# Performance work log

Hardware: AMD Instinct MI355X
Metric: run time of the kernel (lower is better)

The kernel has to match this reference:

```python
import jax, jax.numpy as jnp
import numpy as np

N = 8192
FEAT = 128
HID = 128
EMB = 128
NHEADS = 2
RO_HID = 256
G_EMB = 128
ALPHA = 0.2          # LeakyReLU negative slope
NEG_INF = -9e15      # matches -9000000000000000.0 in the torch source


def _xavier(k, shape, gain=1.0):
    fan_in, fan_out = shape[-2], shape[-1]
    s = gain * np.sqrt(2.0 / (fan_in + fan_out))
    return jax.random.normal(k, shape, jnp.float32) * jnp.float32(s)


def setup_inputs() -> dict:
    key = jax.random.key(0)
    ks = jax.random.split(key, 10)
    adj = jax.random.randint(ks[0], (N, N), 0, 2, jnp.int32)          # dense 0/1 adjacency
    x = jax.random.normal(ks[1], (N, FEAT), jnp.float32)
    W_heads = _xavier(ks[2], (NHEADS, FEAT, HID), gain=1.414)
    a_heads = _xavier(ks[3], (NHEADS, 2 * HID, 1), gain=1.414)
    W_out = _xavier(ks[4], (NHEADS * HID, EMB), gain=1.414)
    a_out = _xavier(ks[5], (2 * EMB, 1), gain=1.414)
    ge_w1 = _xavier(ks[6], (FEAT + EMB, RO_HID))
    ge_b1 = jnp.zeros((RO_HID,), jnp.float32)
    ge_w2 = _xavier(ks[7], (RO_HID, G_EMB))
    ge_b2 = jnp.zeros((G_EMB,), jnp.float32)
    return dict(adj=adj, feature_matrix=x, W_heads=W_heads, a_heads=a_heads,
                W_out=W_out, a_out=a_out, ge_w1=ge_w1, ge_b1=ge_b1,
                ge_w2=ge_w2, ge_b2=ge_b2, supply=0)


def _gat_layer(x, mask, W, a, concat):
    # Faithful to GraphAttentionLayer: e_ij = leakyrelu([Wh_i || Wh_j] @ a).
    # The concat-then-matmul decomposes exactly as Wh@a[:F] + (Wh@a[F:])^T,
    # avoiding the O(N^2 * 2F) a_input tensor while computing identical math.
    Wh = x @ W                                   # [N, F]
    F_out = W.shape[1]
    f1 = (Wh @ a[:F_out]).squeeze(-1)            # [N]
    f2 = (Wh @ a[F_out:]).squeeze(-1)            # [N]
    e = jax.nn.leaky_relu(f1[:, None] + f2[None, :], ALPHA)   # [N, N]
    e = jnp.where(mask, e, jnp.float32(NEG_INF))
    att = jax.nn.softmax(e, axis=1)              # dropout is identity in eval mode
    h = att @ Wh                                 # [N, F]
    return jax.nn.elu(h) if concat else h


def reference(adj, feature_matrix, W_heads, a_heads, W_out, a_out,
              ge_w1, ge_b1, ge_w2, ge_b2, supply):
    mask = adj > 0
    # GAT: multi-head layer 1 (concat), then out_att (no concat) + elu
    heads = [_gat_layer(feature_matrix, mask, W_heads[i], a_heads[i], True)
             for i in range(NHEADS)]
    h = jnp.concatenate(heads, axis=1)           # [N, NHEADS*HID]
    node_emb = jax.nn.elu(_gat_layer(h, mask, W_out, a_out, False))  # [N, EMB]
    # GraphEmb readout (mode='mean')
    combined = jnp.concatenate([feature_matrix, node_emb], axis=1)   # [N, FEAT+EMB]
    h1 = jax.nn.relu(combined @ ge_w1 + ge_b1)
    h2 = jax.nn.relu(h1 @ ge_w2 + ge_b2)
    graph_emb = jnp.mean(h2, axis=0)             # [G_EMB]
    return node_emb, graph_emb
```

## Files before the change

kernel.cpp:

```cpp
#include <hip/hip_runtime.h>
#include <hip/hip_bf16.h>

typedef unsigned short u16;
typedef __attribute__((ext_vector_type(4))) float f32x4;
typedef __attribute__((ext_vector_type(8))) short bf16x8;
typedef __attribute__((ext_vector_type(4))) unsigned short u16x4;

#define N 8192
#define LOG2E 1.4426950408889634f

__device__ __forceinline__ float bf2f(u16 u){
  union { float f; unsigned int i; } v; v.i = ((unsigned int)u) << 16; return v.f;
}
__device__ __forceinline__ u16 f2bf(float f){
  union { float f; unsigned int i; } v; v.f = f;
  unsigned int r = v.i + 0x7fffu + ((v.i >> 16) & 1u);
  return (u16)(r >> 16);
}
__device__ __forceinline__ f32x4 mfma16(bf16x8 a, bf16x8 b, f32x4 c){
  return __builtin_amdgcn_mfma_f32_16x16x32_bf16(a, b, c, 0, 0, 0);
}
__device__ __forceinline__ unsigned int fkey_enc(float f){
  unsigned int u = __float_as_uint(f);
  return (u & 0x80000000u) ? ~u : (u | 0x80000000u);
}
__device__ __forceinline__ float fkey_dec(unsigned int k){
  unsigned int u = (k & 0x80000000u) ? (k ^ 0x80000000u) : ~k;
  return __uint_as_float(u);
}
__device__ __forceinline__ void gload16(const void* g, void* l){
  __builtin_amdgcn_global_load_lds(
      (const __attribute__((address_space(1))) unsigned int*)(g),
      (__attribute__((address_space(3))) unsigned int*)(l), 16, 0, 0);
}

__global__ __launch_bounds__(256) void k_pack(const int* __restrict__ adj,
                                              unsigned long long* __restrict__ packed){
  const int wid = blockIdx.x * 4 + (threadIdx.x >> 6);
  const int lane = threadIdx.x & 63;
  const size_t base = (size_t)wid * 128;
  #pragma unroll 4
  for (int g = 0; g < 128; ++g){
    const size_t grp = base + g;
    const int v = adj[grp * 64 + lane];
    const unsigned long long m = __ballot(v != 0);
    if (lane == 0) packed[grp] = m;
  }
}

__global__ __launch_bounds__(256) void k_prep(
    const float* __restrict__ x, const float* __restrict__ Wh, const float* __restrict__ Wo,
    const float* __restrict__ g1, const float* __restrict__ g2,
    const float* __restrict__ ah, const float* __restrict__ ao,
    u16* __restrict__ xbf, u16* __restrict__ comb,
    u16* __restrict__ wth, u16* __restrict__ wot,
    u16* __restrict__ g1t, u16* __restrict__ g2t,
    float* __restrict__ wa, unsigned int* __restrict__ fkey, float* __restrict__ csum)
{
  const int b = blockIdx.x, t = threadIdx.x;
  if (b < 1024){
    const int idx = b * 256 + t;
    f32x4 v = ((const f32x4*)x)[idx];
    u16x4 h;
    #pragma unroll
    for (int e = 0; e < 4; ++e) h[e] = f2bf(v[e]);
    ((u16x4*)xbf)[idx] = h;
    const int i = idx >> 5, c4 = (idx & 31) * 4;
    *(u16x4*)(comb + (size_t)i * 256 + c4) = h;
  } else if (b < 1152){
    const int rel = (b - 1024) * 256 + t;
    const int head = rel >> 14, win = rel & 16383;
    const int n = win >> 7, k = win & 127;
    wth[rel] = f2bf(Wh[(head << 14) + k * 128 + n]);
  } else if (b < 1280){
    const int rel = (b - 1152) * 256 + t;
    const int n = rel >> 8, k = rel & 255;
    wot[rel] = f2bf(Wo[k * 128 + n]);
  } else if (b < 1536){
    const int rel = (b - 1280) * 256 + t;
    const int n = rel >> 8, k = rel & 255;
    g1t[rel] = f2bf(g1[k * 256 + n]);
  } else if (b < 1664){
    const int rel = (b - 1536) * 256 + t;
    const int n = rel >> 8, k = rel & 255;
    g2t[rel] = f2bf(g2[k * 128 + n]);
  } else if (b < 1667){
    const int z = b - 1664;
    if (z < 2){
      if (t < 128){
        float a1 = 0.f, a2 = 0.f;
        for (int c = 0; c < 128; ++c){
          const float w = Wh[(size_t)z * 16384 + t * 128 + c];
          a1 += w * ah[z * 256 + c];
          a2 += w * ah[z * 256 + 128 + c];
        }
        wa[z * 128 + t] = a1; wa[256 + z * 128 + t] = a2;
      }
    } else {
      if (t < 256){
        float a1 = 0.f, a2 = 0.f;
        for (int c = 0; c < 128; ++c){
          const float w = Wo[(size_t)t * 128 + c];
          a1 += w * ao[c];
          a2 += w * ao[128 + c];
        }
        wa[512 + t] = a1; wa[768 + t] = a2;
      }
    }
  } else {
    if (t < 128) csum[t] = 0.f;
    if (t < 4) fkey[t] = 0u;
  }
}

__global__ __launch_bounds__(256) void k_gemv1(const float* __restrict__ x, const float* __restrict__ wa,
                                               float* __restrict__ f1s, float* __restrict__ f2s,
                                               unsigned int* __restrict__ fkey){
  const int h = blockIdx.y;
  const float* wa1 = wa + h * 128;
  const float* wa2 = wa + 256 + h * 128;
  const int lane = threadIdx.x & 63, w = threadIdx.x >> 6;
  const int r16 = lane & 15, g4 = lane >> 4;
  const int row = blockIdx.x * 16 + w * 4 + g4;
  const float* xr = x + (size_t)row * 128 + r16 * 8;
  f32x4 x0 = *(const f32x4*)(xr);
  f32x4 x1 = *(const f32x4*)(xr + 4);
  f32x4 wA0 = *(const f32x4*)(wa1 + r16 * 8);
  f32x4 wA1 = *(const f32x4*)(wa1 + r16 * 8 + 4);
  f32x4 wB0 = *(const f32x4*)(wa2 + r16 * 8);
  f32x4 wB1 = *(const f32x4*)(wa2 + r16 * 8 + 4);
  float d1 = 0.f, d2 = 0.f;
  #pragma unroll
  for (int e = 0; e < 4; ++e){
    d1 += x0[e] * wA0[e] + x1[e] * wA1[e];
    d2 += x0[e] * wB0[e] + x1[e] * wB1[e];
  }
  d1 += __shfl_xor(d1, 1); d1 += __shfl_xor(d1, 2); d1 += __shfl_xor(d1, 4); d1 += __shfl_xor(d1, 8);
  d2 += __shfl_xor(d2, 1); d2 += __shfl_xor(d2, 2); d2 += __shfl_xor(d2, 4); d2 += __shfl_xor(d2, 8);
  const float d1s = d1 * LOG2E, d2s = d2 * LOG2E;
  if (r16 == 0){
    f1s[(size_t)h * N + row] = d1s;
    f2s[(size_t)h * N + row] = d2s;
  }
  float m = d2s;
  m = fmaxf(m, __shfl_xor(m, 16)); m = fmaxf(m, __shfl_xor(m, 32));
  if (lane == 0) atomicMax(fkey + h, fkey_enc(m));
}

__global__ __launch_bounds__(256) void k_gemv2(const u16* __restrict__ hbf,
                                               const float* __restrict__ wao1, const float* __restrict__ wao2,
                                               float* __restrict__ f1s, float* __restrict__ f2s,
                                               unsigned int* __restrict__ fkey){
  const int lane = threadIdx.x & 63, w = threadIdx.x >> 6;
  const int r16 = lane & 15, g4 = lane >> 4;
  const int row = blockIdx.x * 16 + w * 4 + g4;
  bf16x8 h0 = *(const bf16x8*)(hbf + (size_t)row * 256 + r16 * 16);
  bf16x8 h1 = *(const bf16x8*)(hbf + (size_t)row * 256 + r16 * 16 + 8);
  float d1 = 0.f, d2 = 0.f;
  #pragma unroll
  for (int e = 0; e < 8; ++e){
    const float v0 = bf2f((u16)h0[e]), v1 = bf2f((u16)h1[e]);
    d1 += v0 * wao1[r16 * 16 + e] + v1 * wao1[r16 * 16 + 8 + e];
    d2 += v0 * wao2[r16 * 16 + e] + v1 * wao2[r16 * 16 + 8 + e];
  }
  d1 += __shfl_xor(d1, 1); d1 += __shfl_xor(d1, 2); d1 += __shfl_xor(d1, 4); d1 += __shfl_xor(d1, 8);
  d2 += __shfl_xor(d2, 1); d2 += __shfl_xor(d2, 2); d2 += __shfl_xor(d2, 4); d2 += __shfl_xor(d2, 8);
  const float d1s = d1 * LOG2E, d2s = d2 * LOG2E;
  if (r16 == 0){
    f1s[row] = d1s;
    f2s[row] = d2s;
  }
  float m = d2s;
  m = fmaxf(m, __shfl_xor(m, 16)); m = fmaxf(m, __shfl_xor(m, 32));
  if (lane == 0) atomicMax(fkey, fkey_enc(m));
}

__global__ __launch_bounds__(256) void k_gemm_at(const u16* __restrict__ A_all, const u16* __restrict__ B,
                                                 u16* __restrict__ outT_all, int K){
  const int head = blockIdx.y;
  const u16* A = A_all + (size_t)head * 128 * K;
  u16* outT = outT_all + (size_t)head * 1048576;
  const int lane = threadIdx.x & 63, w = threadIdx.x >> 6;
  const int r16 = lane & 15, g4 = lane >> 4;
  const size_t ib = (size_t)blockIdx.x * 64 + w * 16;
  f32x4 acc[8];
  #pragma unroll
  for (int cg = 0; cg < 8; ++cg) acc[cg] = (f32x4){0,0,0,0};
  for (int kk = 0; kk < K; kk += 32){
    bf16x8 b = *(const bf16x8*)(B + (ib + r16) * (size_t)K + kk + g4 * 8);
    #pragma unroll
    for (int cg = 0; cg < 8; ++cg){
      bf16x8 a = *(const bf16x8*)(A + (size_t)(cg * 16 + r16) * K + kk + g4 * 8);
      acc[cg] = mfma16(a, b, acc[cg]);
    }
  }
  const int jp = w * 16 + r16;
  u16* tb = outT + (size_t)blockIdx.x * 8192;
  #pragma unroll
  for (int cg = 0; cg < 8; ++cg)
    #pragma unroll
    for (int q = 0; q < 4; ++q){
      const int c = cg * 16 + g4 * 4 + q;
      tb[c * 64 + (jp ^ ((c & 7) << 3))] = f2bf(acc[cg][q]);
    }
}

template<int S>
__global__ __launch_bounds__(256, 4) void k_attn(
    const unsigned char* __restrict__ pk,
    const u16* __restrict__ whT_all,
    const float* __restrict__ f1_all, const float* __restrict__ f2_all,
    const unsigned int* __restrict__ fkey,
    u16* __restrict__ part, float* __restrict__ pl)
{
  __shared__ __align__(16) u16 tile[2][8192];
  const int h = blockIdx.z;
  const int s = blockIdx.y;
  const float* f2 = f2_all + (size_t)h * N;
  const float fmax = fkey_dec(fkey[h]);
  const int w = threadIdx.x >> 6;
  const int lane = threadIdx.x & 63;
  const int r16 = lane & 15, g4 = lane >> 4;
  const size_t ibase = (size_t)blockIdx.x * 128 + w * 32;
  constexpr int TPS = 128 / S;
  const int t0 = s * TPS, t1 = t0 + TPS;
  const char* gt = (const char*)whT_all + (size_t)h * 2097152;

  float c1[2], c2[2], lsum[2];
  f32x4 acc[2][8];
  #pragma unroll
  for (int rg = 0; rg < 2; ++rg){
    const float f1v = f1_all[(size_t)h * N + ibase + rg * 16 + r16];
    const float y = f1v + fmax;
    const float mrow = fmaxf(y, 0.2f * y);
    c1[rg] = f1v - mrow;
    c2[rg] = fmaf(0.2f, f1v, -mrow);
    lsum[rg] = 0.f;
    #pragma unroll
    for (int ct = 0; ct < 8; ++ct) acc[rg][ct] = (f32x4){0,0,0,0};
  }

  const int swz = (r16 & 7) << 3;
  const int off0 = r16 * 64 + ((g4 * 8) ^ swz);
  const int off1 = r16 * 64 + ((32 | (g4 * 8)) ^ swz);

  auto stage = [&](int buf, int tt){
    const char* src = gt + (size_t)tt * 16384 + w * 4096 + lane * 16;
    char* dst = ((char*)&tile[0][0]) + buf * 16384 + w * 4096;
    #pragma unroll
    for (int k = 0; k < 4; ++k)
      gload16(src + k * 1024, dst + k * 1024);
  };

  stage(0, t0);
  for (int t = t0; t < t1; ++t){
    const int cur = (t - t0) & 1;
    __syncthreads();
    if (t + 1 < t1) stage(cur ^ 1, t + 1);
    const int j0 = t * 64;
    float fs[16];
    *(f32x4*)&fs[0]  = *(const f32x4*)(f2 + j0 + g4 * 8);
    *(f32x4*)&fs[4]  = *(const f32x4*)(f2 + j0 + g4 * 8 + 4);
    *(f32x4*)&fs[8]  = *(const f32x4*)(f2 + j0 + 32 + g4 * 8);
    *(f32x4*)&fs[12] = *(const f32x4*)(f2 + j0 + 32 + g4 * 8 + 4);
    unsigned int bits[2][2];
    #pragma unroll
    for (int rg = 0; rg < 2; ++rg){
      const size_t rb = (ibase + rg * 16 + r16) * 1024 + t * 8;
      bits[rg][0] = pk[rb + g4];
      bits[rg][1] = pk[rb + 4 + g4];
    }
    bf16x8 pa[2][2];
    #pragma unroll
    for (int rg = 0; rg < 2; ++rg){
      #pragma unroll
      for (int k2 = 0; k2 < 2; ++k2){
        float pv[8];
        #pragma unroll
        for (int x = 0; x < 8; ++x){
          const float sv = fs[k2 * 8 + x];
          const float p = __builtin_amdgcn_exp2f(fmaxf(sv + c1[rg], fmaf(sv, 0.2f, c2[rg])));
          pv[x] = ((bits[rg][k2] >> x) & 1u) ? p : 0.f;
          lsum[rg] += pv[x];
        }
        union { __hip_bfloat162 h2[4]; bf16x8 v8; } u;
        u.h2[0] = __float22bfloat162_rn(make_float2(pv[0], pv[1]));
        u.h2[1] = __float22bfloat162_rn(make_float2(pv[2], pv[3]));
        u.h2[2] = __float22bfloat162_rn(make_float2(pv[4], pv[5]));
        u.h2[3] = __float22bfloat162_rn(make_float2(pv[6], pv[7]));
        pa[rg][k2] = u.v8;
      }
    }
    const u16* lp = &tile[cur][0];
    #pragma unroll
    for (int ct = 0; ct < 8; ++ct){
      bf16x8 b0 = *(const bf16x8*)(lp + off0 + ct * 1024);
      acc[0][ct] = mfma16(pa[0][0], b0, acc[0][ct]);
      acc[1][ct] = mfma16(pa[1][0], b0, acc[1][ct]);
    }
    #pragma unroll
    for (int ct = 0; ct < 8; ++ct){
      bf16x8 b1 = *(const bf16x8*)(lp + off1 + ct * 1024);
      acc[0][ct] = mfma16(pa[0][1], b1, acc[0][ct]);
      acc[1][ct] = mfma16(pa[1][1], b1, acc[1][ct]);
    }
  }

  const int plane = h * S + s;
  u16* pp = part + (size_t)plane * (size_t)(N * 128);
  #pragma unroll
  for (int rg = 0; rg < 2; ++rg){
    float lv = lsum[rg];
    lv += __shfl_xor(lv, 16); lv += __shfl_xor(lv, 32);
    if (lane < 16) pl[(size_t)plane * N + ibase + rg * 16 + lane] = lv;
    #pragma unroll
    for (int ct = 0; ct < 8; ++ct)
      #pragma unroll
      for (int q = 0; q < 4; ++q)
        pp[(ibase + rg * 16 + g4 * 4 + q) * 128 + ct * 16 + r16] = f2bf(acc[rg][ct][q]);
  }
}

template<int S, bool L2>
__global__ __launch_bounds__(256) void k_attn_merge(
    const u16* __restrict__ part, const float* __restrict__ pl,
    u16* __restrict__ hbf, float* __restrict__ nodeout, u16* __restrict__ comb)
{
  const int h = blockIdx.y;
  const int idx = blockIdx.x * 256 + threadIdx.x;
  const int i = idx >> 5, c4 = (idx & 31) * 4;
  f32x4 a = (f32x4){0,0,0,0};
  float L = 0.f;
  #pragma unroll
  for (int s = 0; s < S; ++s){
    const size_t plane = h * S + s;
    u16x4 v = *(const u16x4*)(part + plane * (size_t)(N * 128) + (size_t)i * 128 + c4);
    a[0] += bf2f(v[0]); a[1] += bf2f(v[1]); a[2] += bf2f(v[2]); a[3] += bf2f(v[3]);
    L += pl[plane * (size_t)N + i];
  }
  const float linv = 1.f / L;
  u16x4 hv;
  #pragma unroll
  for (int e = 0; e < 4; ++e){
    float o = a[e] * linv;
    o = (o > 0.f) ? o : (__expf(o) - 1.f);
    a[e] = o;
    hv[e] = f2bf(o);
  }
  if constexpr (!L2){
    *(u16x4*)(hbf + (size_t)i * 256 + h * 128 + c4) = hv;
  } else {
    *(f32x4*)(nodeout + (size_t)i * 128 + c4) = a;
    *(u16x4*)(comb + (size_t)i * 256 + 128 + c4) = hv;
  }
}

template<bool STORE, bool COLSUM>
__global__ __launch_bounds__(256) void k_gemm_row(
    const u16* __restrict__ A, const u16* __restrict__ BT,
    const float* __restrict__ bias,
    u16* __restrict__ out, float* __restrict__ csum,
    int K, int Ntot)
{
  const int lane = threadIdx.x & 63, w = threadIdx.x >> 6;
  const int r16 = lane & 15, g4 = lane >> 4;
  const size_t rbase = (size_t)blockIdx.x * 64 + w * 16;
  const int cbase = blockIdx.y * 128;
  f32x4 acc[8];
  #pragma unroll
  for (int ct = 0; ct < 8; ++ct) acc[ct] = (f32x4){0,0,0,0};
  for (int kk = 0; kk < K; kk += 32){
    bf16x8 af = *(const bf16x8*)(A + (rbase + r16) * (size_t)K + kk + g4 * 8);
    #pragma unroll
    for (int ct = 0; ct < 8; ++ct){
      bf16x8 bfr = *(const bf16x8*)(BT + (size_t)(cbase + ct * 16 + r16) * K + kk + g4 * 8);
      acc[ct] = mfma16(af, bfr, acc[ct]);
    }
  }
  #pragma unroll
  for (int ct = 0; ct < 8; ++ct){
    const float bv = bias[cbase + ct * 16 + r16];
    float sacc = 0.f;
    #pragma unroll
    for (int q = 0; q < 4; ++q){
      float v = acc[ct][q] + bv;
      v = fmaxf(v, 0.f);
      if constexpr (STORE)
        out[(rbase + g4 * 4 + q) * (size_t)Ntot + cbase + ct * 16 + r16] = f2bf(v);
      sacc += v;
    }
    if constexpr (COLSUM){
      sacc += __shfl_xor(sacc, 16); sacc += __shfl_xor(sacc, 32);
      if (lane < 16) atomicAdd(&csum[cbase + ct * 16 + lane], sacc);
    }
  }
}

__global__ void k_final(const float* __restrict__ csum, float* __restrict__ out){
  out[threadIdx.x] = csum[threadIdx.x] * (1.f / 8192.f);
}

extern "C" void kernel_launch(void* const* d_in, const int* in_sizes, int n_in,
                              void* d_out, int out_size, void* d_ws, size_t ws_size,
                              hipStream_t stream) {
  const int*   adj = (const int*)d_in[0];
  const float* x   = (const float*)d_in[1];
  const float* Wh  = (const float*)d_in[2];
  const float* ah  = (const float*)d_in[3];
  const float* Wo  = (const float*)d_in[4];
  const float* ao  = (const float*)d_in[5];
  const float* g1  = (const float*)d_in[6];
  const float* b1  = (const float*)d_in[7];
  const float* g2  = (const float*)d_in[8];
  const float* b2  = (const float*)d_in[9];
  float* outp = (float*)d_out;
  char* ws = (char*)d_ws;

  constexpr size_t PK   = 0;
  constexpr size_t PART = 8388608;
  constexpr size_t PL   = 41943040;
  constexpr size_t XBF  = 42467328;
  constexpr size_t WHT1 = 44564480;
  constexpr size_t WHT2 = 48758784;
  constexpr size_t HBF  = 50855936;
  constexpr size_t COMB = 55050240;
  constexpr size_t H1RO = WHT1;
  constexpr size_t F1S  = 59244544;
  constexpr size_t F2S  = 59310080;
  constexpr size_t CSUM = 59375616;
  constexpr size_t WTH  = 59376128;
  constexpr size_t WOT  = 59441664;
  constexpr size_t G1T  = 59507200;
  constexpr size_t G2T  = 59638272;
  constexpr size_t WA   = 59703808;
  constexpr size_t FKEY = 59707904;

  k_pack<<<2048, 256, 0, stream>>>(adj, (unsigned long long*)(ws + PK));
  k_prep<<<1668, 256, 0, stream>>>(x, Wh, Wo, g1, g2, ah, ao,
      (u16*)(ws + XBF), (u16*)(ws + COMB), (u16*)(ws + WTH), (u16*)(ws + WOT),
      (u16*)(ws + G1T), (u16*)(ws + G2T),
      (float*)(ws + WA), (unsigned int*)(ws + FKEY), (float*)(ws + CSUM));

  k_gemv1<<<dim3(512, 2), 256, 0, stream>>>(x, (const float*)(ws + WA),
      (float*)(ws + F1S), (float*)(ws + F2S), (unsigned int*)(ws + FKEY));
  k_gemm_at<<<dim3(128, 2), 256, 0, stream>>>((const u16*)(ws + WTH), (const u16*)(ws + XBF),
                                              (u16*)(ws + WHT1), 128);
  k_attn<8><<<dim3(64, 8, 2), 256, 0, stream>>>(
      (const unsigned char*)(ws + PK), (const u16*)(ws + WHT1),
      (const float*)(ws + F1S), (const float*)(ws + F2S), (const unsigned int*)(ws + FKEY),
      (u16*)(ws + PART), (float*)(ws + PL));
  k_attn_merge<8, false><<<dim3(1024, 2), 256, 0, stream>>>(
      (const u16*)(ws + PART), (const float*)(ws + PL),
      (u16*)(ws + HBF), nullptr, nullptr);

  k_gemv2<<<dim3(512, 1), 256, 0, stream>>>((const u16*)(ws + HBF),
      (const float*)(ws + WA) + 512, (const float*)(ws + WA) + 768,
      (float*)(ws + F1S), (float*)(ws + F2S), (unsigned int*)(ws + FKEY) + 2);
  k_gemm_at<<<dim3(128, 1), 256, 0, stream>>>((const u16*)(ws + WOT), (const u16*)(ws + HBF),
                                              (u16*)(ws + WHT2), 256);
  k_attn<16><<<dim3(64, 16, 1), 256, 0, stream>>>(
      (const unsigned char*)(ws + PK), (const u16*)(ws + WHT2),
      (const float*)(ws + F1S), (const float*)(ws + F2S), (const unsigned int*)(ws + FKEY) + 2,
      (u16*)(ws + PART), (float*)(ws + PL));
  k_attn_merge<16, true><<<dim3(1024, 1), 256, 0, stream>>>(
      (const u16*)(ws + PART), (const float*)(ws + PL),
      nullptr, outp, (u16*)(ws + COMB));

  k_gemm_row<true, false><<<dim3(128, 2), 256, 0, stream>>>(
      (const u16*)(ws + COMB), (const u16*)(ws + G1T), b1,
      (u16*)(ws + H1RO), nullptr, 256, 256);
  k_gemm_row<false, true><<<dim3(128, 1), 256, 0, stream>>>(
      (const u16*)(ws + H1RO), (const u16*)(ws + G2T), b2,
      nullptr, (float*)(ws + CSUM), 256, 128);
  k_final<<<1, 128, 0, stream>>>((const float*)(ws + CSUM), outp + (size_t)N * 128);
}
```

Measured before the change: 690.2 us.

## Interleave packed mask bits, halve attention splits, tile-layout partial outputs

The adjacency bitmask is byte-permuted at pack time so each lane reads its mask bits as one 16-bit load instead of several byte loads. The attention loop is restructured to process one k-half at a time, which lowers register pressure, and launch bounds drop to 2 waves per SIMD. The split count is halved for both layers (8→4, 16→8), which halves the partial-sum planes and merge traffic but gives fewer blocks to fill the GPU. Partial outputs are written in a lane-contiguous tiled layout that the merge kernel reads with matching index math, making the attention stores coalesced.

Measured after the change: 703.2 us. About the same (+1.9%).

```diff
diff --git a/kernel.cpp b/kernel.cpp
--- a/kernel.cpp
+++ b/kernel.cpp
@@ -44,7 +44,12 @@
     const size_t grp = base + g;
     const int v = adj[grp * 64 + lane];
     const unsigned long long m = __ballot(v != 0);
-    if (lane == 0) packed[grp] = m;
+    if (lane == 0){
+      const unsigned int lo = (unsigned int)m, hi = (unsigned int)(m >> 32);
+      const unsigned int olo = __builtin_amdgcn_perm(hi, lo, 0x05010400u);
+      const unsigned int ohi = __builtin_amdgcn_perm(hi, lo, 0x07030602u);
+      packed[grp] = ((unsigned long long)ohi << 32) | olo;
+    }
   }
 }
 
@@ -206,7 +211,7 @@
 }
 
 template<int S>
-__global__ __launch_bounds__(256, 4) void k_attn(
+__global__ __launch_bounds__(256, 2) void k_attn(
     const unsigned char* __restrict__ pk,
     const u16* __restrict__ whT_all,
     const float* __restrict__ f1_all, const float* __restrict__ f2_all,
@@ -242,7 +247,8 @@
 
   const int swz = (r16 & 7) << 3;
   const int off0 = r16 * 64 + ((g4 * 8) ^ swz);
-  const int off1 = r16 * 64 + ((32 | (g4 * 8)) ^ swz);
+  const unsigned char* pkr0 = pk + (ibase + r16) * 1024 + g4 * 2;
+  const unsigned char* pkr1 = pkr0 + 16 * 1024;
 
   auto stage = [&](int buf, int tt){
     const char* src = gt + (size_t)tt * 16384 + w * 4096 + lane * 16;
@@ -257,67 +263,70 @@
     const int cur = (t - t0) & 1;
     __syncthreads();
     if (t + 1 < t1) stage(cur ^ 1, t + 1);
-    const int j0 = t * 64;
-    float fs[16];
-    *(f32x4*)&fs[0]  = *(const f32x4*)(f2 + j0 + g4 * 8);
-    *(f32x4*)&fs[4]  = *(const f32x4*)(f2 + j0 + g4 * 8 + 4);
-    *(f32x4*)&fs[8]  = *(const f32x4*)(f2 + j0 + 32 + g4 * 8);
-    *(f32x4*)&fs[12] = *(const f32x4*)(f2 + j0 + 32 + g4 * 8 + 4);
-    unsigned int bits[2][2];
-    #pragma unroll
-    for (int rg = 0; rg < 2; ++rg){
-      const size_t rb = (ibase + rg * 16 + r16) * 1024 + t * 8;
-      bits[rg][0] = pk[rb + g4];
-      bits[rg][1] = pk[rb + 4 + g4];
-    }
-    bf16x8 pa[2][2];
-    #pragma unroll
-    for (int rg = 0; rg < 2; ++rg){
+    const unsigned int bits0 = *(const unsigned short*)(pkr0 + t * 8);
+    const unsigned int bits1 = *(const unsigned short*)(pkr1 + t * 8);
+    const u16* lp = &tile[cur][0];
+    #pragma unroll
+    for (int k2 = 0; k2 < 2; ++k2){
+      const float* fjp = f2 + t * 64 + k2 * 32 + g4 * 8;
+      f32x4 fa = *(const f32x4*)(fjp);
+      f32x4 fb = *(const f32x4*)(fjp + 4);
+      bf16x8 pa0, pa1;
+      {
+        const unsigned int bb = (bits0 >> (k2 * 8)) & 0xFFu;
+        union { __hip_bfloat162 h2[4]; bf16x8 v8; } u;
+        #pragma unroll
+        for (int xp = 0; xp < 4; ++xp){
+          const float s0 = (xp < 2) ? fa[2 * xp] : fb[2 * xp - 4];
+          const float s1 = (xp < 2) ? fa[2 * xp + 1] : fb[2 * xp - 3];
+          float p0 = __builtin_amdgcn_exp2f(fmaxf(s0 + c1[0], fmaf(s0, 0.2f, c2[0])));
+          float p1 = __builtin_amdgcn_exp2f(fmaxf(s1 + c1[0], fmaf(s1, 0.2f, c2[0])));
+          p0 = ((bb >> (2 * xp)) & 1u) ? p0 : 0.f;
+          p1 = ((bb >> (2 * xp + 1)) & 1u) ? p1 : 0.f;
+          lsum[0] += p0 + p1;
+          u.h2[xp] = __float22bfloat162_rn(make_float2(p0, p1));
+        }
+        pa0 = u.v8;
+      }
+      {
+        const unsigned int bb = (bits1 >> (k2 * 8)) & 0xFFu;
+        union { __hip_bfloat162 h2[4]; bf16x8 v8; } u;
+        #pragma unroll
+        for (int xp = 0; xp < 4; ++xp){
+          const float s0 = (xp < 2) ? fa[2 * xp] : fb[2 * xp - 4];
+          const float s1 = (xp < 2) ? fa[2 * xp + 1] : fb[2 * xp - 3];
+          float p0 = __builtin_amdgcn_exp2f(fmaxf(s0 + c1[1], fmaf(s0, 0.2f, c2[1])));
+          float p1 = __builtin_amdgcn_exp2f(fmaxf(s1 + c1[1], fmaf(s1, 0.2f, c2[1])));
+          p0 = ((bb >> (2 * xp)) & 1u) ? p0 : 0.f;
+          p1 = ((bb >> (2 * xp + 1)) & 1u) ? p1 : 0.f;
+          lsum[1] += p0 + p1;
+          u.h2[xp] = __float22bfloat162_rn(make_float2(p0, p1));
+        }
+        pa1 = u.v8;
+      }
+      const int offk = off0 ^ (k2 << 5);
       #pragma unroll
-      for (int k2 = 0; k2 < 2; ++k2){
-        float pv[8];
-        #pragma unroll
-        for (int x = 0; x < 8; ++x){
-          const float sv = fs[k2 * 8 + x];
-          const float p = __builtin_amdgcn_exp2f(fmaxf(sv + c1[rg], fmaf(sv, 0.2f, c2[rg])));
-          pv[x] = ((bits[rg][k2] >> x) & 1u) ? p : 0.f;
-          lsum[rg] += pv[x];
-        }
-        union { __hip_bfloat162 h2[4]; bf16x8 v8; } u;
-        u.h2[0] = __float22bfloat162_rn(make_float2(pv[0], pv[1]));
-        u.h2[1] = __float22bfloat162_rn(make_float2(pv[2], pv[3]));
-        u.h2[2] = __float22bfloat162_rn(make_float2(pv[4], pv[5]));
-        u.h2[3] = __float22bfloat162_rn(make_float2(pv[6], pv[7]));
-        pa[rg][k2] = u.v8;
+      for (int ct = 0; ct < 8; ++ct){
+        bf16x8 b = *(const bf16x8*)(lp + offk + ct * 1024);
+        acc[0][ct] = mfma16(pa0, b, acc[0][ct]);
+        acc[1][ct] = mfma16(pa1, b, acc[1][ct]);
       }
     }
-    const u16* lp = &tile[cur][0];
-    #pragma unroll
-    for (int ct = 0; ct < 8; ++ct){
-      bf16x8 b0 = *(const bf16x8*)(lp + off0 + ct * 1024);
-      acc[0][ct] = mfma16(pa[0][0], b0, acc[0][ct]);
-      acc[1][ct] = mfma16(pa[1][0], b0, acc[1][ct]);
-    }
-    #pragma unroll
-    for (int ct = 0; ct < 8; ++ct){
-      bf16x8 b1 = *(const bf16x8*)(lp + off1 + ct * 1024);
-      acc[0][ct] = mfma16(pa[0][1], b1, acc[0][ct]);
-      acc[1][ct] = mfma16(pa[1][1], b1, acc[1][ct]);
-    }
   }
 
   const int plane = h * S + s;
-  u16* pp = part + (size_t)plane * (size_t)(N * 128);
   #pragma unroll
   for (int rg = 0; rg < 2; ++rg){
+    const int tile_row = (int)(ibase >> 4) + rg;
+    u16* pp = part + ((size_t)plane * 512 + tile_row) * 2048;
+    #pragma unroll
+    for (int ct = 0; ct < 8; ++ct)
+      #pragma unroll
+      for (int q = 0; q < 4; ++q)
+        pp[(ct * 4 + q) * 64 + lane] = f2bf(acc[rg][ct][q]);
     float lv = lsum[rg];
     lv += __shfl_xor(lv, 16); lv += __shfl_xor(lv, 32);
     if (lane < 16) pl[(size_t)plane * N + ibase + rg * 16 + lane] = lv;
-    #pragma unroll
-    for (int ct = 0; ct < 8; ++ct)
-      #pragma unroll
-      for (int q = 0; q < 4; ++q)
-        pp[(ibase + rg * 16 + g4 * 4 + q) * 128 + ct * 16 + r16] = f2bf(acc[rg][ct][q]);
   }
 }
 
@@ -329,12 +338,14 @@
   const int h = blockIdx.y;
   const int idx = blockIdx.x * 256 + threadIdx.x;
   const int i = idx >> 5, c4 = (idx & 31) * 4;
+  const int tl = i >> 4, r = i & 15;
+  const size_t off = (size_t)tl * 2048 + (size_t)(((c4 >> 4) * 4 + (r & 3)) * 64 + ((r >> 2) & 3) * 16 + (c4 & 15));
   f32x4 a = (f32x4){0,0,0,0};
   float L = 0.f;
   #pragma unroll
   for (int s = 0; s < S; ++s){
     const size_t plane = h * S + s;
-    u16x4 v = *(const u16x4*)(part + plane * (size_t)(N * 128) + (size_t)i * 128 + c4);
+    u16x4 v = *(const u16x4*)(part + plane * (size_t)(N * 128) + off);
     a[0] += bf2f(v[0]); a[1] += bf2f(v[1]); a[2] += bf2f(v[2]); a[3] += bf2f(v[3]);
     L += pl[plane * (size_t)N + i];
   }
@@ -418,22 +429,22 @@
 
   constexpr size_t PK   = 0;
   constexpr size_t PART = 8388608;
-  constexpr size_t PL   = 41943040;
-  constexpr size_t XBF  = 42467328;
-  constexpr size_t WHT1 = 44564480;
-  constexpr size_t WHT2 = 48758784;
-  constexpr size_t HBF  = 50855936;
-  constexpr size_t COMB = 55050240;
+  constexpr size_t PL   = 25165824;
+  constexpr size_t XBF  = 25427968;
+  constexpr size_t WHT1 = 27525120;
+  constexpr size_t WHT2 = 31719424;
+  constexpr size_t HBF  = 33816576;
+  constexpr size_t COMB = 38010880;
   constexpr size_t H1RO = WHT1;
-  constexpr size_t F1S  = 59244544;
-  constexpr size_t F2S  = 59310080;
-  constexpr size_t CSUM = 59375616;
-  constexpr size_t WTH  = 59376128;
-  constexpr size_t WOT  = 59441664;
-  constexpr size_t G1T  = 59507200;
-  constexpr size_t G2T  = 59638272;
-  constexpr size_t WA   = 59703808;
-  constexpr size_t FKEY = 59707904;
+  constexpr size_t F1S  = 42205184;
+  constexpr size_t F2S  = 42270720;
+  constexpr size_t CSUM = 42336256;
+  constexpr size_t WTH  = 42336768;
+  constexpr size_t WOT  = 42402304;
+  constexpr size_t G1T  = 42467840;
+  constexpr size_t G2T  = 42598912;
+  constexpr size_t WA   = 42664448;
+  constexpr size_t FKEY = 42668544;
 
   k_pack<<<2048, 256, 0, stream>>>(adj, (unsigned long long*)(ws + PK));
   k_prep<<<1668, 256, 0, stream>>>(x, Wh, Wo, g1, g2, ah, ao,
@@ -445,11 +456,11 @@
       (float*)(ws + F1S), (float*)(ws + F2S), (unsigned int*)(ws + FKEY));
   k_gemm_at<<<dim3(128, 2), 256, 0, stream>>>((const u16*)(ws + WTH), (const u16*)(ws + XBF),
                                               (u16*)(ws + WHT1), 128);
-  k_attn<8><<<dim3(64, 8, 2), 256, 0, stream>>>(
+  k_attn<4><<<dim3(64, 4, 2), 256, 0, stream>>>(
       (const unsigned char*)(ws + PK), (const u16*)(ws + WHT1),
       (const float*)(ws + F1S), (const float*)(ws + F2S), (const unsigned int*)(ws + FKEY),
       (u16*)(ws + PART), (float*)(ws + PL));
-  k_attn_merge<8, false><<<dim3(1024, 2), 256, 0, stream>>>(
+  k_attn_merge<4, false><<<dim3(1024, 2), 256, 0, stream>>>(
       (const u16*)(ws + PART), (const float*)(ws + PL),
       (u16*)(ws + HBF), nullptr, nullptr);
 
@@ -458,11 +469,11 @@
       (float*)(ws + F1S), (float*)(ws + F2S), (unsigned int*)(ws + FKEY) + 2);
   k_gemm_at<<<dim3(128, 1), 256, 0, stream>>>((const u16*)(ws + WOT), (const u16*)(ws + HBF),
                                               (u16*)(ws + WHT2), 256);
-  k_attn<16><<<dim3(64, 16, 1), 256, 0, stream>>>(
+  k_attn<8><<<dim3(64, 8, 1), 256, 0, stream>>>(
       (const unsigned char*)(ws + PK), (const u16*)(ws + WHT2),
       (const float*)(ws + F1S), (const float*)(ws + F2S), (const unsigned int*)(ws + FKEY) + 2,
       (u16*)(ws + PART), (float*)(ws + PL));
-  k_attn_merge<16, true><<<dim3(1024, 1), 256, 0, stream>>>(
+  k_attn_merge<8, true><<<dim3(1024, 1), 256, 0, stream>>>(
       (const u16*)(ws + PART), (const float*)(ws + PL),
       nullptr, outp, (u16*)(ws + COMB));
 
```
